# Optimization experiments

Measured on AMD Instinct MI355X. Metric: run time of the kernel, lower is better.

Reference implementation:

```python
import jax, jax.numpy as jnp
import numpy as np

K = 20
NEG = jnp.float32(-1e30)

def _l2norm(x):
    # F.normalize(x, dim=1, p=2) with eps clamp
    n = jnp.sqrt(jnp.sum(x * x, axis=1, keepdims=True))
    return x / jnp.maximum(n, 1e-12)

def setup_inputs() -> dict:
    key = jax.random.key(0)
    k1, k2, k3 = jax.random.split(key, 3)
    h, w, C = 96, 96, 256
    query_label = jax.random.randint(k1, (h, w, 3), 0, 2, dtype=jnp.int64)
    color = jnp.zeros((3,), dtype=jnp.int64)
    q_feat = jax.random.normal(k2, (1, C, h, w), dtype=jnp.float32)
    s_feat = jax.random.normal(k3, (1, C, h, w), dtype=jnp.float32)
    return {"query_label": query_label, "color": color, "q_feat": q_feat, "s_feat": s_feat}

def reference(query_label, color, q_feat, s_feat):
    C = q_feat.shape[1]
    out_hw = s_feat.shape[2:]
    # mask at feature resolution (query_label already sized [h,w,3])
    mask = jnp.all(query_label == color, axis=-1).reshape(-1)      # [M]
    q = q_feat[0].transpose(1, 2, 0).reshape(-1, C)                # [M,C]
    s = s_feat[0].transpose(1, 2, 0).reshape(-1, C)                # [N,C]
    qn = _l2norm(q)
    sn = _l2norm(s)
    sim = sn @ qn.T                                                # [N,M] cosine sims
    # top-K over fg columns == top-K over full row with non-fg masked to -inf
    fg_top = jax.lax.top_k(jnp.where(mask[None, :], sim, NEG), K)[0]
    bg_top = jax.lax.top_k(jnp.where(mask[None, :], NEG, sim), K)[0]
    fg_score = jnp.mean(fg_top, axis=1).reshape(out_hw)
    bg_score = jnp.mean(bg_top, axis=1).reshape(out_hw)
    return fg_score, bg_score
```

## Files before the change

### kernel.cpp

```cpp
#include <hip/hip_runtime.h>
#include <math.h>

#define MTOT 9216
#define CDIM 256
#define KSEL 20
#define NCHUNK 8
#define CHUNKQ 1152
#define BS 32
#define QSTEP 128
#define NSTEP 9
#define NSLAB 36

typedef __attribute__((ext_vector_type(8))) short short8;
typedef __attribute__((ext_vector_type(8))) unsigned short ushort8;
typedef __attribute__((ext_vector_type(4))) float f32x4;
typedef __attribute__((ext_vector_type(2))) _Float16 h2;

__device__ __forceinline__ unsigned short f2bf(float v) {
    unsigned u = __float_as_uint(v);
    u += 0x7FFF + ((u >> 16) & 1);
    return (unsigned short)(u >> 16);
}
__device__ __forceinline__ h2 pkh2(float lo, float hi) {
    auto r = __builtin_amdgcn_cvt_pkrtz(lo, hi);
    h2 h; __builtin_memcpy(&h, &r, 4); return h;
}
__device__ __forceinline__ h2 asH2(unsigned int u) {
    h2 h; __builtin_memcpy(&h, &u, 4); return h;
}
__device__ __forceinline__ unsigned int h2u(h2 h) {
    unsigned int u; __builtin_memcpy(&u, &h, 4); return u;
}
__device__ __forceinline__ h2 h2max(h2 a, h2 b) {
    h2 d; asm("v_pk_max_f16 %0, %1, %2" : "=v"(d) : "v"(a), "v"(b)); return d;
}
__device__ __forceinline__ h2 h2min(h2 a, h2 b) {
    h2 d; asm("v_pk_min_f16 %0, %1, %2" : "=v"(d) : "v"(a), "v"(b)); return d;
}
__device__ __forceinline__ unsigned short hbits(_Float16 x) {
    unsigned short u; __builtin_memcpy(&u, &x, 2); return u;
}
__device__ __forceinline__ float hs2f(unsigned short u) {
    _Float16 x; __builtin_memcpy(&x, &u, 2); return (float)x;
}

__device__ __forceinline__ void ins20p(h2 (&l)[KSEL], h2 v) {
    v = h2max(v, l[0]);
#pragma unroll
    for (int i = 0; i < KSEL - 1; ++i) {
        h2 nxt = l[i + 1];
        l[i] = h2min(nxt, v);
        v = h2max(nxt, v);
    }
    l[KSEL - 1] = v;
}
__device__ __forceinline__ void ins20(float (&l)[KSEL], float v) {
#pragma unroll
    for (int i = 0; i < KSEL - 1; ++i) {
        float nxt = l[i + 1];
        l[i] = fminf(nxt, v);
        v = fmaxf(nxt, v);
    }
    l[KSEL - 1] = v;
}

__global__ __launch_bounds__(256) void prepconv_kernel(
    const int* __restrict__ ql, const int* __restrict__ color,
    const float* __restrict__ qf, const float* __restrict__ sf,
    int* __restrict__ cnt,
    unsigned short* __restrict__ qbt, unsigned short* __restrict__ sbt)
{
    __shared__ float tilef[32 * 257];
    __shared__ float red[256];
    __shared__ float invv[32];
    __shared__ int slotl[32];
    const int bid = blockIdx.x;
    const bool isQ = bid < (MTOT / 32);
    const int m0 = (isQ ? bid : bid - MTOT / 32) * 32;
    const float* src = isQ ? qf : sf;
    const int t = threadIdx.x;
    const int ml = t & 31, cb = t >> 5;
    float sq = 0.f;
#pragma unroll
    for (int i = 0; i < 32; ++i) {
        int c = cb * 32 + i;
        float v = src[c * MTOT + m0 + ml];
        tilef[ml * 257 + c] = v;
        sq += v * v;
    }
    red[cb * 32 + ml] = sq;
    __syncthreads();
    if (t < 32) {
        float s = 0.f;
#pragma unroll
        for (int j = 0; j < 8; ++j) s += red[j * 32 + t];
        invv[t] = 1.0f / fmaxf(sqrtf(s), 1e-12f);
        if (isQ) {
            int m = m0 + t;
            bool fg = (ql[3*m] == color[0]) & (ql[3*m+1] == color[1]) & (ql[3*m+2] == color[2]);
            slotl[t] = fg ? atomicAdd(&cnt[0], 1) : (MTOT - 1 - atomicAdd(&cnt[1], 1));
        }
    }
    __syncthreads();
    const int row = t >> 3, seg = t & 7;
    const float iv = invv[row];
    const int drow = isQ ? slotl[row] : (m0 + row);
    unsigned short* dst = (isQ ? qbt : sbt) + (size_t)drow * 256 + seg * 32;
    const float* srcr = &tilef[row * 257 + seg * 32];
#pragma unroll
    for (int ch = 0; ch < 4; ++ch) {
        ushort8 o;
#pragma unroll
        for (int e = 0; e < 8; ++e) o[e] = f2bf(srcr[ch * 8 + e] * iv);
        *(ushort8*)(dst + ch * 8) = o;
    }
}

__global__ __launch_bounds__(256, 3) void matchsim_kernel(
    const unsigned short* __restrict__ qbt, const unsigned short* __restrict__ sbt,
    const int* __restrict__ cnt, unsigned short* __restrict__ part)
{
    __shared__ __align__(16) char smem[49152];
    unsigned int* mbuf = (unsigned int*)smem;

    const int t = threadIdx.x;
    const int w = t >> 6, l = t & 63;
    const int sblk = blockIdx.x >> 3;
    const int chunk = blockIdx.x & 7;
    const int s0 = sblk * BS;
    const int q0c = chunk * CHUNKQ;
    const int fgc = cnt[0];

    {
        int row = t >> 3, cb = t & 7;
        const ushort8* gs = (const ushort8*)(sbt + (size_t)(s0 + row) * 256);
#pragma unroll
        for (int i = 0; i < 4; ++i) {
            int ch = cb + i * 8;
            ushort8 v = gs[ch];
            int byte = (row * 512 + ch * 16) ^ ((row & 7) << 4);
            *(ushort8*)(smem + byte) = v;
        }
    }
    __syncthreads();

    const h2 NEG2 = { (_Float16)-65504.f, (_Float16)-65504.f };
    h2 fgl[KSEL], bgl[KSEL];
#pragma unroll
    for (int i = 0; i < KSEL; ++i) { fgl[i] = NEG2; bgl[i] = NEG2; }

    const int wl = (t & 63) >> 1;
    const int qhalf = t & 1;
    auto loadQ = [&](int gslab, ushort8 (&dst)[4]) {
        int step = gslab >> 2, slab = gslab & 3;
        const unsigned short* base =
            qbt + (size_t)(q0c + step * QSTEP + w * 32 + wl) * 256 + slab * 64 + qhalf * 32;
#pragma unroll
        for (int i = 0; i < 4; ++i)
            dst[i] = *(const ushort8*)(base + i * 8);
    };
    ushort8 qrA[4], qrB[4];
    loadQ(0, qrA);
    loadQ(1, qrB);
    const int qwswz = (wl & 7) << 4;
    char* const qbase = smem + 16384 + w * 4096;

    const int lg = l >> 4;
    const int aq0 = l & 15;
    const int aq1 = aq0 + 16;
    const int aswz0 = (aq0 & 7) << 4, aswz1 = (aq1 & 7) << 4;
    const int srow0 = l & 15, srow1 = srow0 + 16;
    const int bswz0 = (srow0 & 7) << 4, bswz1 = (srow1 & 7) << 4;

    f32x4 acc00 = {0,0,0,0}, acc01 = {0,0,0,0}, acc10 = {0,0,0,0}, acc11 = {0,0,0,0};
    int cur = 0;

    auto slabBody = [&](int gslab, ushort8 (&stash)[4]) {
        char* Qs = qbase + cur * 16384;
#pragma unroll
        for (int i = 0; i < 4; ++i) {
            int byte = (wl * 128 + qhalf * 64 + i * 16) ^ qwswz;
            *(ushort8*)(Qs + byte) = stash[i];
        }
        if (gslab + 2 < NSLAB) loadQ(gslab + 2, stash);
        const int slab = gslab & 3;
        __builtin_amdgcn_s_setprio(1);
#pragma unroll
        for (int ks = 0; ks < 2; ++ks) {
            int ak = ks * 64 + lg * 16;
            short8 a0 = *(const short8*)(Qs + ((aq0 * 128 + ak) ^ aswz0));
            short8 a1 = *(const short8*)(Qs + ((aq1 * 128 + ak) ^ aswz1));
            int bk = slab * 128 + ks * 64 + lg * 16;
            short8 b0 = *(const short8*)(smem + ((srow0 * 512 + bk) ^ bswz0));
            short8 b1 = *(const short8*)(smem + ((srow1 * 512 + bk) ^ bswz1));
            acc00 = __builtin_amdgcn_mfma_f32_16x16x32_bf16(a0, b0, acc00, 0, 0, 0);
            acc01 = __builtin_amdgcn_mfma_f32_16x16x32_bf16(a0, b1, acc01, 0, 0, 0);
            acc10 = __builtin_amdgcn_mfma_f32_16x16x32_bf16(a1, b0, acc10, 0, 0, 0);
            acc11 = __builtin_amdgcn_mfma_f32_16x16x32_bf16(a1, b1, acc11, 0, 0, 0);
        }
        __builtin_amdgcn_s_setprio(0);
        cur ^= 1;
        if (slab == 3) {
            const int step = gslab >> 2;
            const int qw0 = q0c + step * QSTEP + w * 32;
#pragma unroll
            for (int qt = 0; qt < 2; ++qt) {
                const f32x4& aS0 = qt ? acc10 : acc00;
                const f32x4& aS1 = qt ? acc11 : acc01;
                int qfirst = qw0 + qt * 16;
                if (qfirst + 16 <= fgc) {
#pragma unroll
                    for (int r = 0; r < 4; ++r) ins20p(fgl, pkh2(aS0[r], aS1[r]));
                } else if (qfirst >= fgc) {
#pragma unroll
                    for (int r = 0; r < 4; ++r) ins20p(bgl, pkh2(aS0[r], aS1[r]));
                } else {
#pragma unroll
                    for (int r = 0; r < 4; ++r) {
                        h2 v = pkh2(aS0[r], aS1[r]);
                        bool m = (qfirst + lg * 4 + r) < fgc;
                        ins20p(fgl, m ? v : NEG2);
                        ins20p(bgl, m ? NEG2 : v);
                    }
                }
            }
            acc00 = (f32x4){0,0,0,0}; acc01 = (f32x4){0,0,0,0};
            acc10 = (f32x4){0,0,0,0}; acc11 = (f32x4){0,0,0,0};
        }
    };

    for (int gs = 0; gs < NSLAB; gs += 2) {
        slabBody(gs,     qrA);
        slabBody(gs + 1, qrB);
    }

    __syncthreads();
    const int sp = l & 15, owner = w * 4 + lg;
    auto midx = [](int cls, int own, int spi) { return ((cls * 16 + own) * 16 + spi) * 21; };
    {
        unsigned int* df = &mbuf[midx(0, owner, sp)];
        unsigned int* db = &mbuf[midx(1, owner, sp)];
#pragma unroll
        for (int k = 0; k < KSEL; ++k) { df[k] = h2u(fgl[k]); db[k] = h2u(bgl[k]); }
    }
    __syncthreads();
    auto mergeL = [&](unsigned int* A, const unsigned int* B) {
        h2 la[KSEL];
#pragma unroll
        for (int k = 0; k < KSEL; ++k) la[k] = asH2(A[k]);
        for (int j = KSEL - 1; j >= 0; --j) {
            h2 v = asH2(B[j]);
            if (!(v.x > la[0].x || v.y > la[0].y)) break;
            ins20p(la, v);
        }
#pragma unroll
        for (int k = 0; k < KSEL; ++k) A[k] = h2u(la[k]);
    };
    {
        int cls = t >> 7, u = t & 127, spi = u & 15, j = u >> 4;
        mergeL(&mbuf[midx(cls, j, spi)], &mbuf[midx(cls, j + 8, spi)]);
    }
    __syncthreads();
    if (t < 128) {
        int cls = t >> 6, u = t & 63, spi = u & 15, j = u >> 4;
        mergeL(&mbuf[midx(cls, j, spi)], &mbuf[midx(cls, j + 4, spi)]);
    }
    __syncthreads();
    if (t < 64) {
        int cls = t >> 5, u = t & 31, spi = u & 15, j = u >> 4;
        mergeL(&mbuf[midx(cls, j, spi)], &mbuf[midx(cls, j + 2, spi)]);
    }
    __syncthreads();
    if (t < 32) {
        int cls = t >> 4, spi = t & 15;
        unsigned int* A = &mbuf[midx(cls, 0, spi)];
        const unsigned int* B = &mbuf[midx(cls, 1, spi)];
        h2 la[KSEL];
#pragma unroll
        for (int k = 0; k < KSEL; ++k) la[k] = asH2(A[k]);
        for (int j = KSEL - 1; j >= 0; --j) {
            h2 v = asH2(B[j]);
            if (!(v.x > la[0].x || v.y > la[0].y)) break;
            ins20p(la, v);
        }
        unsigned short* d0 = &part[((size_t)(s0 + spi)      * NCHUNK + chunk) * (2*KSEL) + cls*KSEL];
        unsigned short* d1 = &part[((size_t)(s0 + 16 + spi) * NCHUNK + chunk) * (2*KSEL) + cls*KSEL];
#pragma unroll
        for (int k = 0; k < KSEL; ++k) {
            d0[k] = hbits(la[k].x);
            d1[k] = hbits(la[k].y);
        }
    }
}

__global__ __launch_bounds__(256) void finalize_kernel(
    const unsigned short* __restrict__ part, float* __restrict__ out)
{
    int idx = blockIdx.x * 256 + threadIdx.x;
    if (idx >= 2 * MTOT) return;
    int n = idx >> 1, cls = idx & 1;
    const unsigned short* base = part + (size_t)n * NCHUNK * 2 * KSEL + cls * KSEL;
    float la[KSEL];
#pragma unroll
    for (int k = 0; k < KSEL; ++k) la[k] = hs2f(base[k]);
    for (int ch = 1; ch < NCHUNK; ++ch) {
        const unsigned short* sp = base + ch * 2 * KSEL;
        for (int j = KSEL - 1; j >= 0; --j) {
            float v = hs2f(sp[j]);
            if (v <= la[0]) break;
            ins20(la, v);
        }
    }
    float s = 0.f;
#pragma unroll
    for (int k = 0; k < KSEL; ++k) s += la[k];
    out[cls * MTOT + n] = s * (1.0f / KSEL);
}

extern "C" void kernel_launch(void* const* d_in, const int* in_sizes, int n_in,
                              void* d_out, int out_size, void* d_ws, size_t ws_size,
                              hipStream_t stream) {
    const int*   ql    = (const int*)d_in[0];
    const int*   color = (const int*)d_in[1];
    const float* qf    = (const float*)d_in[2];
    const float* sf    = (const float*)d_in[3];
    float* out = (float*)d_out;

    int* cnt = (int*)d_ws;
    unsigned short* qbt = (unsigned short*)(cnt + 4);
    unsigned short* sbt = qbt + (size_t)MTOT * CDIM;
    unsigned short* part = sbt + (size_t)MTOT * CDIM;

    (void)hipMemsetAsync(cnt, 0, 16, stream);
    prepconv_kernel<<<2 * (MTOT / 32), 256, 0, stream>>>(ql, color, qf, sf, cnt, qbt, sbt);
    matchsim_kernel<<<(MTOT / BS) * NCHUNK, 256, 0, stream>>>(qbt, sbt, cnt, part);
    finalize_kernel<<<(2 * MTOT + 255) / 256, 256, 0, stream>>>(part, out);
}
```

Baseline: 180.4 us.

## Stream Q tiles straight into LDS with global_load_lds double buffering

Q slabs are now copied from global memory directly into per-wave LDS buffers with 16-byte global_load_lds DMA. This replaces the old path that loaded them into registers and then wrote them to LDS with ds_write. The XOR swizzle moves to the global address side, and the loop keeps one slab in flight, using explicit s_waitcnt vmcnt and a sched_barrier. The aim is to cut VGPR pressure and LDS store instructions. The cost is a shallower prefetch (one slab ahead instead of two) and tighter, manually counted waits on memory operations.

```diff
diff --git a/kernel.cpp b/kernel.cpp
--- a/kernel.cpp
+++ b/kernel.cpp
@@ -42,6 +42,11 @@
 }
 __device__ __forceinline__ float hs2f(unsigned short u) {
     _Float16 x; __builtin_memcpy(&x, &u, 2); return (float)x;
+}
+__device__ __forceinline__ void gl_lds16(const void* g, void* l) {
+    __builtin_amdgcn_global_load_lds(
+        (const __attribute__((address_space(1))) void*)g,
+        (__attribute__((address_space(3))) void*)l, 16, 0, 0);
 }
 
 __device__ __forceinline__ void ins20p(h2 (&l)[KSEL], h2 v) {
@@ -149,21 +154,19 @@
 #pragma unroll
     for (int i = 0; i < KSEL; ++i) { fgl[i] = NEG2; bgl[i] = NEG2; }
 
-    const int wl = (t & 63) >> 1;
-    const int qhalf = t & 1;
-    auto loadQ = [&](int gslab, ushort8 (&dst)[4]) {
+    const int rowAdd = (l >> 3) * 512 + ((((l & 7) ^ ((l >> 3) & 7))) << 4);
+    char* const qbase = smem + 16384 + w * 4096;
+    const char* const qgb = (const char*)qbt;
+    auto dmaQ = [&](int gslab) {
         int step = gslab >> 2, slab = gslab & 3;
-        const unsigned short* base =
-            qbt + (size_t)(q0c + step * QSTEP + w * 32 + wl) * 256 + slab * 64 + qhalf * 32;
-#pragma unroll
-        for (int i = 0; i < 4; ++i)
-            dst[i] = *(const ushort8*)(base + i * 8);
+        const char* bg = qgb + (size_t)(q0c + step * QSTEP + w * 32) * 512
+                             + slab * 128 + rowAdd;
+        char* lb = qbase + (gslab & 1) * 16384;
+#pragma unroll
+        for (int j = 0; j < 4; ++j)
+            gl_lds16(bg + j * 4096, lb + j * 1024);
     };
-    ushort8 qrA[4], qrB[4];
-    loadQ(0, qrA);
-    loadQ(1, qrB);
-    const int qwswz = (wl & 7) << 4;
-    char* const qbase = smem + 16384 + w * 4096;
+    dmaQ(0);
 
     const int lg = l >> 4;
     const int aq0 = l & 15;
@@ -173,16 +176,16 @@
     const int bswz0 = (srow0 & 7) << 4, bswz1 = (srow1 & 7) << 4;
 
     f32x4 acc00 = {0,0,0,0}, acc01 = {0,0,0,0}, acc10 = {0,0,0,0}, acc11 = {0,0,0,0};
-    int cur = 0;
-
-    auto slabBody = [&](int gslab, ushort8 (&stash)[4]) {
-        char* Qs = qbase + cur * 16384;
-#pragma unroll
-        for (int i = 0; i < 4; ++i) {
-            int byte = (wl * 128 + qhalf * 64 + i * 16) ^ qwswz;
-            *(ushort8*)(Qs + byte) = stash[i];
-        }
-        if (gslab + 2 < NSLAB) loadQ(gslab + 2, stash);
+
+    for (int gslab = 0; gslab < NSLAB; ++gslab) {
+        if (gslab + 1 < NSLAB) {
+            dmaQ(gslab + 1);
+            asm volatile("s_waitcnt vmcnt(4)" ::: "memory");
+        } else {
+            asm volatile("s_waitcnt vmcnt(0)" ::: "memory");
+        }
+        __builtin_amdgcn_sched_barrier(0);
+        char* Qs = qbase + (gslab & 1) * 16384;
         const int slab = gslab & 3;
         __builtin_amdgcn_s_setprio(1);
 #pragma unroll
@@ -199,7 +202,6 @@
             acc11 = __builtin_amdgcn_mfma_f32_16x16x32_bf16(a1, b1, acc11, 0, 0, 0);
         }
         __builtin_amdgcn_s_setprio(0);
-        cur ^= 1;
         if (slab == 3) {
             const int step = gslab >> 2;
             const int qw0 = q0c + step * QSTEP + w * 32;
@@ -227,11 +229,6 @@
             acc00 = (f32x4){0,0,0,0}; acc01 = (f32x4){0,0,0,0};
             acc10 = (f32x4){0,0,0,0}; acc11 = (f32x4){0,0,0,0};
         }
-    };
-
-    for (int gs = 0; gs < NSLAB; gs += 2) {
-        slabBody(gs,     qrA);
-        slabBody(gs + 1, qrB);
     }
 
     __syncthreads();
```

Result: slower. 186.8 us (+3.6%).

## Split per-lane top-K lists into two independent chains per query tile

Applied to the files above, without the earlier changes.

Each lane now keeps separate top-20 fg/bg lists for the two 16-query subtiles, so the two insertion sequences are independent and can interleave, shortening the serial dependency chain in the selection phase. The block-level merge tree gains a level to fold the doubled lists and runs once per class, with extra barriers. This doubles the register footprint for the lists (80 packed h2 values), which risks lower occupancy or spills.

```diff
diff --git a/kernel.cpp b/kernel.cpp
--- a/kernel.cpp
+++ b/kernel.cpp
@@ -145,9 +145,11 @@
     __syncthreads();
 
     const h2 NEG2 = { (_Float16)-65504.f, (_Float16)-65504.f };
-    h2 fgl[KSEL], bgl[KSEL];
-#pragma unroll
-    for (int i = 0; i < KSEL; ++i) { fgl[i] = NEG2; bgl[i] = NEG2; }
+    h2 fglA[KSEL], bglA[KSEL], fglB[KSEL], bglB[KSEL];
+#pragma unroll
+    for (int i = 0; i < KSEL; ++i) {
+        fglA[i] = NEG2; bglA[i] = NEG2; fglB[i] = NEG2; bglB[i] = NEG2;
+    }
 
     const int wl = (t & 63) >> 1;
     const int qhalf = t & 1;
@@ -174,6 +176,25 @@
 
     f32x4 acc00 = {0,0,0,0}, acc01 = {0,0,0,0}, acc10 = {0,0,0,0}, acc11 = {0,0,0,0};
     int cur = 0;
+
+    auto selQT = [&](const f32x4& aS0, const f32x4& aS1, int qfirst,
+                     h2 (&fl)[KSEL], h2 (&bl)[KSEL]) {
+        if (qfirst + 16 <= fgc) {
+#pragma unroll
+            for (int r = 0; r < 4; ++r) ins20p(fl, pkh2(aS0[r], aS1[r]));
+        } else if (qfirst >= fgc) {
+#pragma unroll
+            for (int r = 0; r < 4; ++r) ins20p(bl, pkh2(aS0[r], aS1[r]));
+        } else {
+#pragma unroll
+            for (int r = 0; r < 4; ++r) {
+                h2 v = pkh2(aS0[r], aS1[r]);
+                bool m = (qfirst + lg * 4 + r) < fgc;
+                ins20p(fl, m ? v : NEG2);
+                ins20p(bl, m ? NEG2 : v);
+            }
+        }
+    };
 
     auto slabBody = [&](int gslab, ushort8 (&stash)[4]) {
         char* Qs = qbase + cur * 16384;
@@ -203,27 +224,8 @@
         if (slab == 3) {
             const int step = gslab >> 2;
             const int qw0 = q0c + step * QSTEP + w * 32;
-#pragma unroll
-            for (int qt = 0; qt < 2; ++qt) {
-                const f32x4& aS0 = qt ? acc10 : acc00;
-                const f32x4& aS1 = qt ? acc11 : acc01;
-                int qfirst = qw0 + qt * 16;
-                if (qfirst + 16 <= fgc) {
-#pragma unroll
-                    for (int r = 0; r < 4; ++r) ins20p(fgl, pkh2(aS0[r], aS1[r]));
-                } else if (qfirst >= fgc) {
-#pragma unroll
-                    for (int r = 0; r < 4; ++r) ins20p(bgl, pkh2(aS0[r], aS1[r]));
-                } else {
-#pragma unroll
-                    for (int r = 0; r < 4; ++r) {
-                        h2 v = pkh2(aS0[r], aS1[r]);
-                        bool m = (qfirst + lg * 4 + r) < fgc;
-                        ins20p(fgl, m ? v : NEG2);
-                        ins20p(bgl, m ? NEG2 : v);
-                    }
-                }
-            }
+            selQT(acc00, acc01, qw0,      fglA, bglA);
+            selQT(acc10, acc11, qw0 + 16, fglB, bglB);
             acc00 = (f32x4){0,0,0,0}; acc01 = (f32x4){0,0,0,0};
             acc10 = (f32x4){0,0,0,0}; acc11 = (f32x4){0,0,0,0};
         }
@@ -235,15 +237,8 @@
     }
 
     __syncthreads();
+
     const int sp = l & 15, owner = w * 4 + lg;
-    auto midx = [](int cls, int own, int spi) { return ((cls * 16 + own) * 16 + spi) * 21; };
-    {
-        unsigned int* df = &mbuf[midx(0, owner, sp)];
-        unsigned int* db = &mbuf[midx(1, owner, sp)];
-#pragma unroll
-        for (int k = 0; k < KSEL; ++k) { df[k] = h2u(fgl[k]); db[k] = h2u(bgl[k]); }
-    }
-    __syncthreads();
     auto mergeL = [&](unsigned int* A, const unsigned int* B) {
         h2 la[KSEL];
 #pragma unroll
@@ -256,41 +251,57 @@
 #pragma unroll
         for (int k = 0; k < KSEL; ++k) A[k] = h2u(la[k]);
     };
+    auto midx = [](int own, int spi) { return (own * 16 + spi) * 21; };
+    auto mergeTree = [&](int cls) {
+        __syncthreads();
+        {
+            int spi = t & 15, j = t >> 4;
+            mergeL(&mbuf[midx(j, spi)], &mbuf[midx(j + 16, spi)]);
+        }
+        __syncthreads();
+        if (t < 128) { int spi = t & 15, j = t >> 4; mergeL(&mbuf[midx(j, spi)], &mbuf[midx(j + 8, spi)]); }
+        __syncthreads();
+        if (t < 64)  { int spi = t & 15, j = t >> 4; mergeL(&mbuf[midx(j, spi)], &mbuf[midx(j + 4, spi)]); }
+        __syncthreads();
+        if (t < 32)  { int spi = t & 15, j = t >> 4; mergeL(&mbuf[midx(j, spi)], &mbuf[midx(j + 2, spi)]); }
+        __syncthreads();
+        if (t < 16) {
+            int spi = t;
+            unsigned int* A = &mbuf[midx(0, spi)];
+            const unsigned int* B = &mbuf[midx(1, spi)];
+            h2 la[KSEL];
+#pragma unroll
+            for (int k = 0; k < KSEL; ++k) la[k] = asH2(A[k]);
+            for (int j = KSEL - 1; j >= 0; --j) {
+                h2 v = asH2(B[j]);
+                if (!(v.x > la[0].x || v.y > la[0].y)) break;
+                ins20p(la, v);
+            }
+            unsigned short* d0 = &part[((size_t)(s0 + spi)      * NCHUNK + chunk) * (2*KSEL) + cls*KSEL];
+            unsigned short* d1 = &part[((size_t)(s0 + 16 + spi) * NCHUNK + chunk) * (2*KSEL) + cls*KSEL];
+#pragma unroll
+            for (int k = 0; k < KSEL; ++k) {
+                d0[k] = hbits(la[k].x);
+                d1[k] = hbits(la[k].y);
+            }
+        }
+        __syncthreads();
+    };
+
     {
-        int cls = t >> 7, u = t & 127, spi = u & 15, j = u >> 4;
-        mergeL(&mbuf[midx(cls, j, spi)], &mbuf[midx(cls, j + 8, spi)]);
-    }
-    __syncthreads();
-    if (t < 128) {
-        int cls = t >> 6, u = t & 63, spi = u & 15, j = u >> 4;
-        mergeL(&mbuf[midx(cls, j, spi)], &mbuf[midx(cls, j + 4, spi)]);
-    }
-    __syncthreads();
-    if (t < 64) {
-        int cls = t >> 5, u = t & 31, spi = u & 15, j = u >> 4;
-        mergeL(&mbuf[midx(cls, j, spi)], &mbuf[midx(cls, j + 2, spi)]);
-    }
-    __syncthreads();
-    if (t < 32) {
-        int cls = t >> 4, spi = t & 15;
-        unsigned int* A = &mbuf[midx(cls, 0, spi)];
-        const unsigned int* B = &mbuf[midx(cls, 1, spi)];
-        h2 la[KSEL];
-#pragma unroll
-        for (int k = 0; k < KSEL; ++k) la[k] = asH2(A[k]);
-        for (int j = KSEL - 1; j >= 0; --j) {
-            h2 v = asH2(B[j]);
-            if (!(v.x > la[0].x || v.y > la[0].y)) break;
-            ins20p(la, v);
-        }
-        unsigned short* d0 = &part[((size_t)(s0 + spi)      * NCHUNK + chunk) * (2*KSEL) + cls*KSEL];
-        unsigned short* d1 = &part[((size_t)(s0 + 16 + spi) * NCHUNK + chunk) * (2*KSEL) + cls*KSEL];
-#pragma unroll
-        for (int k = 0; k < KSEL; ++k) {
-            d0[k] = hbits(la[k].x);
-            d1[k] = hbits(la[k].y);
-        }
-    }
+        unsigned int* dA = &mbuf[midx(owner, sp)];
+        unsigned int* dB = &mbuf[midx(owner + 16, sp)];
+#pragma unroll
+        for (int k = 0; k < KSEL; ++k) { dA[k] = h2u(fglA[k]); dB[k] = h2u(fglB[k]); }
+    }
+    mergeTree(0);
+    {
+        unsigned int* dA = &mbuf[midx(owner, sp)];
+        unsigned int* dB = &mbuf[midx(owner + 16, sp)];
+#pragma unroll
+        for (int k = 0; k < KSEL; ++k) { dA[k] = h2u(bglA[k]); dB[k] = h2u(bglB[k]); }
+    }
+    mergeTree(1);
 }
 
 __global__ __launch_bounds__(256) void finalize_kernel(
```

New measurement: 707.8 us. 3.92x slower.
